# Performance work log

Measured on AMD Instinct MI355X. Metric: run time of the kernel, lower is better.

## Reference

```python
import jax, jax.numpy as jnp
import numpy as np

N_COMP = 8
N_BASIS = 16
N_FEATURES = 64
N_CAT = 8
N_CONT = 56
N_UNIQUE = 100
BATCH = 32768
T0, T1 = 0.0, 10.0
SEP = 1e-3  # constants.MIN_TRANSITION_POINT_SEP
SIGNS = np.array([1.0, -1.0, 1.0, -1.0, 1.0, -1.0, 1.0, -1.0], dtype=np.float32)
CONT_IDX = np.arange(N_CONT)
CAT_IDX = np.arange(N_CONT, N_FEATURES)


def _offset():
    # torch_inverse_softplus(avg_interval_per_feature)
    v = (T1 - T0) / N_COMP / (N_FEATURES + 1)
    return float(np.log(np.exp(v) - 1.0))


def setup_inputs():
    key = jax.random.key(0)
    ks = jax.random.split(key, 11)
    off = _offset()
    B = jax.random.normal(ks[0], (BATCH, N_CONT, N_BASIS), jnp.float32)
    codes = jax.random.randint(ks[1], (BATCH, N_CAT), 0, N_UNIQUE)
    B_cat = jax.nn.one_hot(codes, N_UNIQUE, dtype=jnp.float32).reshape(BATCH, N_CAT * N_UNIQUE)
    Wh = jax.random.normal(ks[2], (N_BASIS, N_CONT, N_COMP), jnp.float32) + off
    Wh_cat = jax.random.normal(ks[3], (N_CAT, N_UNIQUE, N_COMP), jnp.float32) + off
    bh = jax.random.normal(ks[4], (N_COMP,), jnp.float32) + off
    Wv = jax.random.normal(ks[5], (N_BASIS, N_CONT, N_COMP), jnp.float32)
    Wv_cat = jax.random.normal(ks[6], (N_CAT, N_UNIQUE, N_COMP), jnp.float32)
    bv = jax.random.normal(ks[7], (N_COMP,), jnp.float32)
    Wic = jax.random.normal(ks[8], (N_BASIS, N_CONT, 1), jnp.float32)
    Wic_cat = jax.random.normal(ks[9], (N_CAT, N_UNIQUE, 1), jnp.float32)
    bic = jax.random.normal(ks[10], (1,), jnp.float32)
    return {"B": B, "B_cat": B_cat, "Wh": Wh, "Wh_cat": Wh_cat, "bh": bh,
            "Wv": Wv, "Wv_cat": Wv_cat, "bv": bv,
            "Wic": Wic, "Wic_cat": Wic_cat, "bic": bic}


def _calculate_gams(B, B_cat, W, W_cat, bias, positive):
    # continuous: per-feature small matmul  (b,i,k) x (k,i,c) -> (b,c,i)
    cont = jnp.einsum('bik,kic->bci', B, W)
    # categorical: one-hot gather expressed as blockwise matmul  (b,f,n) x (f,n,c) -> (b,c,f)
    cat = jnp.einsum('bfn,fnc->bcf', B_cat.reshape(B.shape[0], N_CAT, N_UNIQUE), W_cat)
    c = W.shape[2]
    out = jnp.zeros((B.shape[0], c, N_FEATURES + 1), dtype=B.dtype)
    out = out.at[:, :, CONT_IDX].set(cont)
    out = out.at[:, :, CAT_IDX].set(cat)
    out = out.at[:, :, -1].set(bias[None, :])
    return jax.nn.softplus(out) if positive else out


def reference(B, B_cat, Wh, Wh_cat, bh, Wv, Wv_cat, bv, Wic, Wic_cat, bic):
    H = _calculate_gams(B, B_cat, Wh, Wh_cat, bh, True)      # (b, n_comp, n_feat+1)
    V = _calculate_gams(B, B_cat, Wv, Wv_cat, bv, True)      # (b, n_comp, n_feat+1)
    IC = _calculate_gams(B, B_cat, Wic, Wic_cat, bic, False)  # (b, 1, n_feat+1)
    b = B.shape[0]
    signs = jnp.asarray(SIGNS)
    h_sum = H.sum(-1)   # (b, n_comp) per-segment horizontal increments
    v_sum = V.sum(-1)
    sep = SEP * jnp.arange(1, N_COMP + 1, dtype=B.dtype)
    # sequential cumulative build == prefix sums over the composition axis
    t = jnp.concatenate([jnp.full((b, 1), T0, B.dtype),
                         T0 + jnp.cumsum(h_sum, axis=1) + sep], axis=1)  # (b, n_comp+1)
    x0 = IC.sum(-1)     # (b, 1)
    x = jnp.concatenate([x0, x0 + jnp.cumsum(signs * v_sum, axis=1)], axis=1)
    # bounded composition: clamp the last horizontal coordinate
    t = t.at[:, -1].set(jnp.maximum(t[:, -2] + SEP, T1))
    return jnp.stack([t, x], axis=-1)  # (b, n_comp+1, 2)
```

## Files before the change

kernel.cpp:

```cpp
#include <hip/hip_runtime.h>

#define NCOMP 8
#define NCONT 56
#define NCAT 8
#define NU 100
#define NROWS 32768
#define SEPC 1e-3f
#define T1F 10.0f

typedef __fp16 f16x2 __attribute__((ext_vector_type(2)));
typedef _Float16 h2arith __attribute__((ext_vector_type(2)));

#define FSTRIDE 35

union H8 { f16x2 h2[4]; float4 f4; };

__device__ __forceinline__ float sp(float x) {
    return 0.69314718f * __builtin_amdgcn_logf(1.0f + __builtin_amdgcn_exp2f(x * 1.44269504f));
}

__device__ __forceinline__ f16x2 pkrtz(float a, float b) {
    return __builtin_amdgcn_cvt_pkrtz(a, b);
}

__device__ __forceinline__ float fdot2(f16x2 a, f16x2 b, float c) {
    return __builtin_amdgcn_fdot2(a, b, c, false);
}

__device__ __forceinline__ h2arith h2shfl_xor(h2arith v, int off) {
    int i = __builtin_bit_cast(int, v);
    i = __shfl_xor(i, off, 64);
    return __builtin_bit_cast(h2arith, i);
}

__device__ __forceinline__ void acc_cont(const float4* __restrict__ pw,
                                         float4 a0, float4 a1, float4 a2, float4 a3,
                                         float* sh, float* sw, float& ic) {
    f16x2 ba[8];
    ba[0] = pkrtz(a0.x, a0.y); ba[1] = pkrtz(a0.z, a0.w);
    ba[2] = pkrtz(a1.x, a1.y); ba[3] = pkrtz(a1.z, a1.w);
    ba[4] = pkrtz(a2.x, a2.y); ba[5] = pkrtz(a2.z, a2.w);
    ba[6] = pkrtz(a3.x, a3.y); ba[7] = pkrtz(a3.z, a3.w);
#pragma unroll
    for (int c = 0; c < NCOMP; ++c) {
        H8 u0, u1, v0, v1;
        u0.f4 = pw[2 * c];      u1.f4 = pw[2 * c + 1];
        v0.f4 = pw[16 + 2 * c]; v1.f4 = pw[17 + 2 * c];
        float hA = 0.0f, vA = 0.0f;
#pragma unroll
        for (int p = 0; p < 4; ++p) {
            hA = fdot2(ba[p], u0.h2[p], hA);
            vA = fdot2(ba[p], v0.h2[p], vA);
        }
#pragma unroll
        for (int p = 0; p < 4; ++p) {
            hA = fdot2(ba[4 + p], u1.h2[p], hA);
            vA = fdot2(ba[4 + p], v1.h2[p], vA);
        }
        sh[c] += sp(hA);
        sw[c] += sp(vA);
    }
    H8 i0, i1;
    i0.f4 = pw[32]; i1.f4 = pw[33];
    float iA = 0.0f;
#pragma unroll
    for (int p = 0; p < 4; ++p) iA = fdot2(ba[p], i0.h2[p], iA);
#pragma unroll
    for (int p = 0; p < 4; ++p) iA = fdot2(ba[4 + p], i1.h2[p], iA);
    ic += iA;
}

__global__ __launch_bounds__(512, 4) void tpm_kernel(
    const float* __restrict__ B, const float* __restrict__ Bcat,
    const float* __restrict__ Wh, const float* __restrict__ Whc, const float* __restrict__ bh,
    const float* __restrict__ Wv, const float* __restrict__ Wvc, const float* __restrict__ bv,
    const float* __restrict__ Wic, const float* __restrict__ Wicc, const float* __restrict__ bic,
    float* __restrict__ out)
{
    __shared__ float4 sW[NCONT * FSTRIDE];
    __shared__ float2 sBias[NCOMP];
    __shared__ float  sBic;
    __shared__ int    sCode[8][4][NCAT];

    const int tid = threadIdx.x;

    for (int idx = tid; idx < 896; idx += 512) {
        int icp = idx % 448, t = idx / 448;
        int i = icp >> 3, c = icp & 7;
        const float* gh = Wh + (size_t)(8 * t) * 448 + icp;
        const float* gv = Wv + (size_t)(8 * t) * 448 + icp;
        H8 uh, uv;
#pragma unroll
        for (int p = 0; p < 4; ++p) {
            uh.h2[p] = pkrtz(gh[(2 * p) * 448], gh[(2 * p + 1) * 448]);
            uv.h2[p] = pkrtz(gv[(2 * p) * 448], gv[(2 * p + 1) * 448]);
        }
        sW[i * FSTRIDE + 2 * c + t] = uh.f4;
        sW[i * FSTRIDE + 16 + 2 * c + t] = uv.f4;
    }
    if (tid < 112) {
        int i = tid % 56, t = tid / 56;
        const float* gi = Wic + (size_t)(8 * t) * 56 + i;
        H8 u;
#pragma unroll
        for (int p = 0; p < 4; ++p)
            u.h2[p] = pkrtz(gi[(2 * p) * 56], gi[(2 * p + 1) * 56]);
        sW[i * FSTRIDE + 32 + t] = u.f4;
    }
    if (tid < NCOMP) sBias[tid] = make_float2(sp(bh[tid]), sp(bv[tid]));
    if (tid == NCOMP) sBic = bic[0];
    __syncthreads();

    const int lane = tid & 63;
    const int widx = tid >> 6;
    const int s = lane & 15;
    const int g = lane >> 4;
    const int R0 = (((blockIdx.x << 3) + widx) << 2);
    const int r = R0 + g;
    const float* browp = B + (size_t)r * 896;

    {
        const float4* pc = (const float4*)(Bcat + (size_t)R0 * 800);
#pragma unroll
        for (int it = 0; it < 13; ++it) {
            int idx = it * 64 + lane;
            if (it < 12 || idx < 800) {
                int row = idx / 200;
                int pos = idx - row * 200;
                float4 q = pc[idx];
                float n = (float)(4 * pos);
                float sc = q.x * (n + 1.0f) + q.y * (n + 2.0f) + q.z * (n + 3.0f) + q.w * (n + 4.0f);
                if (sc > 0.5f) {
                    int p = (int)sc - 1;
                    int f = p / NU;
                    sCode[widx][row][f] = p - f * NU;
                }
            }
        }
    }
    __threadfence_block();

    float4 p3a, p3b, p3c, p3d;
    float p3ic = 0.0f;
    if (s >= 8) {
        int fi = s - 8;
        int cc = sCode[widx][g][fi];
        int gA = fi * NU + cc;
        const float4* qh = (const float4*)(Whc + gA * 8);
        const float4* qv = (const float4*)(Wvc + gA * 8);
        p3a = qh[0]; p3b = qh[1]; p3c = qv[0]; p3d = qv[1];
        p3ic = Wicc[gA];
    }

    float sh[NCOMP], sw[NCOMP];
    float ic = 0.0f;
#pragma unroll
    for (int c = 0; c < NCOMP; ++c) { sh[c] = sw[c] = 0.0f; }

    float4 cb0, cb1, cb2, cb3;
    {
        const float4* p = (const float4*)(browp + s * 16);
        cb0 = p[0]; cb1 = p[1]; cb2 = p[2]; cb3 = p[3];
    }

#pragma unroll
    for (int j = 0; j < 3; ++j) {
        float4 nb0, nb1, nb2, nb3;
        if (j < 2) {
            const float4* p = (const float4*)(browp + (s + 16 * (j + 1)) * 16);
            nb0 = p[0]; nb1 = p[1]; nb2 = p[2]; nb3 = p[3];
        } else {
            int f3 = (s < 8) ? (s + 48) : 48;
            const float4* p = (const float4*)(browp + f3 * 16);
            nb0 = p[0]; nb1 = p[1]; nb2 = p[2]; nb3 = p[3];
        }
        acc_cont(sW + (s + 16 * j) * FSTRIDE, cb0, cb1, cb2, cb3, sh, sw, ic);
        cb0 = nb0; cb1 = nb1; cb2 = nb2; cb3 = nb3;
    }

    if (s < 8) {
        acc_cont(sW + (s + 48) * FSTRIDE, cb0, cb1, cb2, cb3, sh, sw, ic);
    } else {
        sh[0] += sp(p3a.x); sh[1] += sp(p3a.y); sh[2] += sp(p3a.z); sh[3] += sp(p3a.w);
        sh[4] += sp(p3b.x); sh[5] += sp(p3b.y); sh[6] += sp(p3b.z); sh[7] += sp(p3b.w);
        sw[0] += sp(p3c.x); sw[1] += sp(p3c.y); sw[2] += sp(p3c.z); sw[3] += sp(p3c.w);
        sw[4] += sp(p3d.x); sw[5] += sp(p3d.y); sw[6] += sp(p3d.z); sw[7] += sp(p3d.w);
        ic += p3ic;
    }

    h2arith hw[NCOMP];
#pragma unroll
    for (int c = 0; c < NCOMP; ++c)
        hw[c] = __builtin_bit_cast(h2arith, pkrtz(sh[c], sw[c]));
#pragma unroll
    for (int off = 8; off >= 1; off >>= 1) {
#pragma unroll
        for (int c = 0; c < NCOMP; ++c)
            hw[c] = hw[c] + h2shfl_xor(hw[c], off);
        ic += __shfl_xor(ic, off, 64);
    }

    if (s < 9) {
        int m = (s == 8) ? 7 : s;
        float tj = SEPC * (float)s;
        float xj = ic + sBic;
#pragma unroll
        for (int c = 0; c < NCOMP; ++c) {
            float2 bb2 = sBias[c];
            if (c < m) tj += (float)hw[c][0] + bb2.x;
            if (c < s) {
                float vv = (float)hw[c][1] + bb2.y;
                xj += (c & 1) ? -vv : vv;
            }
        }
        if (s == 8) tj = fmaxf(tj, T1F);
        float2 o; o.x = tj; o.y = xj;
        ((float2*)out)[(size_t)r * 9 + s] = o;
    }
}

extern "C" void kernel_launch(void* const* d_in, const int* in_sizes, int n_in,
                              void* d_out, int out_size, void* d_ws, size_t ws_size,
                              hipStream_t stream) {
    (void)in_sizes; (void)n_in; (void)out_size; (void)d_ws; (void)ws_size;
    const float* B    = (const float*)d_in[0];
    const float* Bcat = (const float*)d_in[1];
    const float* Wh   = (const float*)d_in[2];
    const float* Whc  = (const float*)d_in[3];
    const float* bh   = (const float*)d_in[4];
    const float* Wv   = (const float*)d_in[5];
    const float* Wvc  = (const float*)d_in[6];
    const float* bv   = (const float*)d_in[7];
    const float* Wic  = (const float*)d_in[8];
    const float* Wicc = (const float*)d_in[9];
    const float* bic  = (const float*)d_in[10];
    float* out = (float*)d_out;

    hipLaunchKernelGGL(tpm_kernel, dim3(1024), dim3(512), 0, stream,
                       B, Bcat, Wh, Whc, bh, Wv, Wvc, bv, Wic, Wicc, bic, out);
}
```

Measured before the change: 260.7 us.

## Precompute fp16 weight tiles in prep kernel and overlap Bcat scan with compute

Adds a small prep kernel that packs the continuous weights into fp16 float4 tiles and the softplus'd biases into the workspace once per call. Each block then just copies that packed layout into shared memory instead of gathering and converting strided weights itself. The one-hot Bcat loads and scan are issued early and interleaved with the continuous-feature accumulation, and the B row loads are software-pipelined. Inside acc_cont the weight reads from shared memory are double-buffered one component ahead. The cost is an extra kernel launch and higher register pressure from keeping many loads in flight.

```diff
diff --git a/kernel.cpp b/kernel.cpp
--- a/kernel.cpp
+++ b/kernel.cpp
@@ -4,14 +4,15 @@
 #define NCONT 56
 #define NCAT 8
 #define NU 100
-#define NROWS 32768
 #define SEPC 1e-3f
 #define T1F 10.0f
 
+#define FSTRIDE 35
+#define WS_NW4 2048
+#define WS_BIAS_OFF 32768
+
 typedef __fp16 f16x2 __attribute__((ext_vector_type(2)));
 typedef _Float16 h2arith __attribute__((ext_vector_type(2)));
-
-#define FSTRIDE 35
 
 union H8 { f16x2 h2[4]; float4 f4; };
 
@@ -41,11 +42,19 @@
     ba[2] = pkrtz(a1.x, a1.y); ba[3] = pkrtz(a1.z, a1.w);
     ba[4] = pkrtz(a2.x, a2.y); ba[5] = pkrtz(a2.z, a2.w);
     ba[6] = pkrtz(a3.x, a3.y); ba[7] = pkrtz(a3.z, a3.w);
+    H8 u0, u1, v0, v1;
+    u0.f4 = pw[0];  u1.f4 = pw[1];
+    v0.f4 = pw[16]; v1.f4 = pw[17];
 #pragma unroll
     for (int c = 0; c < NCOMP; ++c) {
-        H8 u0, u1, v0, v1;
-        u0.f4 = pw[2 * c];      u1.f4 = pw[2 * c + 1];
-        v0.f4 = pw[16 + 2 * c]; v1.f4 = pw[17 + 2 * c];
+        H8 nu0, nu1, nv0, nv1;
+        if (c < NCOMP - 1) {
+            nu0.f4 = pw[2 * c + 2];  nu1.f4 = pw[2 * c + 3];
+            nv0.f4 = pw[18 + 2 * c]; nv1.f4 = pw[19 + 2 * c];
+        } else {
+            nu0.f4 = pw[32]; nu1.f4 = pw[33];
+            nv0.f4 = u0.f4;  nv1.f4 = u1.f4;
+        }
         float hA = 0.0f, vA = 0.0f;
 #pragma unroll
         for (int p = 0; p < 4; ++p) {
@@ -59,58 +68,66 @@
         }
         sh[c] += sp(hA);
         sw[c] += sp(vA);
-    }
-    H8 i0, i1;
-    i0.f4 = pw[32]; i1.f4 = pw[33];
+        u0 = nu0; u1 = nu1; v0 = nv0; v1 = nv1;
+    }
     float iA = 0.0f;
 #pragma unroll
-    for (int p = 0; p < 4; ++p) iA = fdot2(ba[p], i0.h2[p], iA);
-#pragma unroll
-    for (int p = 0; p < 4; ++p) iA = fdot2(ba[4 + p], i1.h2[p], iA);
+    for (int p = 0; p < 4; ++p) iA = fdot2(ba[p], u0.h2[p], iA);
+#pragma unroll
+    for (int p = 0; p < 4; ++p) iA = fdot2(ba[4 + p], u1.h2[p], iA);
     ic += iA;
+}
+
+__global__ __launch_bounds__(512) void prep_kernel(
+    const float* __restrict__ Wh, const float* __restrict__ Wv,
+    const float* __restrict__ Wic, const float* __restrict__ bh,
+    const float* __restrict__ bv, const float* __restrict__ bic,
+    float4* __restrict__ ws)
+{
+    const int id = blockIdx.x * 512 + threadIdx.x;
+    const int i  = id / FSTRIDE;
+    const int rr = id - i * FSTRIDE;
+    H8 u;
+    u.f4 = make_float4(0.f, 0.f, 0.f, 0.f);
+    if (i < NCONT && rr < 34) {
+        if (rr < 32) {
+            const int c = (rr & 15) >> 1;
+            const int t = rr & 1;
+            const float* W  = (rr < 16) ? Wh : Wv;
+            const float* gp = W + (size_t)(8 * t) * 448 + i * 8 + c;
+#pragma unroll
+            for (int p = 0; p < 4; ++p)
+                u.h2[p] = pkrtz(gp[(2 * p) * 448], gp[(2 * p + 1) * 448]);
+        } else {
+            const int t = rr - 32;
+            const float* gp = Wic + (size_t)(8 * t) * 56 + i;
+#pragma unroll
+            for (int p = 0; p < 4; ++p)
+                u.h2[p] = pkrtz(gp[(2 * p) * 56], gp[(2 * p + 1) * 56]);
+        }
+    }
+    ws[id] = u.f4;
+    if (id < NCOMP) {
+        float2* b2 = (float2*)((char*)ws + WS_BIAS_OFF);
+        b2[id] = make_float2(sp(bh[id]), sp(bv[id]));
+    }
+    if (id == NCOMP) {
+        *((float*)((char*)ws + WS_BIAS_OFF + 64)) = bic[0];
+    }
 }
 
 __global__ __launch_bounds__(512, 4) void tpm_kernel(
     const float* __restrict__ B, const float* __restrict__ Bcat,
-    const float* __restrict__ Wh, const float* __restrict__ Whc, const float* __restrict__ bh,
-    const float* __restrict__ Wv, const float* __restrict__ Wvc, const float* __restrict__ bv,
-    const float* __restrict__ Wic, const float* __restrict__ Wicc, const float* __restrict__ bic,
+    const float* __restrict__ Whc, const float* __restrict__ Wvc,
+    const float* __restrict__ Wicc, const float4* __restrict__ ws,
     float* __restrict__ out)
 {
-    __shared__ float4 sW[NCONT * FSTRIDE];
+    __shared__ float4 sW[WS_NW4];
     __shared__ float2 sBias[NCOMP];
     __shared__ float  sBic;
     __shared__ int    sCode[8][4][NCAT];
 
-    const int tid = threadIdx.x;
-
-    for (int idx = tid; idx < 896; idx += 512) {
-        int icp = idx % 448, t = idx / 448;
-        int i = icp >> 3, c = icp & 7;
-        const float* gh = Wh + (size_t)(8 * t) * 448 + icp;
-        const float* gv = Wv + (size_t)(8 * t) * 448 + icp;
-        H8 uh, uv;
-#pragma unroll
-        for (int p = 0; p < 4; ++p) {
-            uh.h2[p] = pkrtz(gh[(2 * p) * 448], gh[(2 * p + 1) * 448]);
-            uv.h2[p] = pkrtz(gv[(2 * p) * 448], gv[(2 * p + 1) * 448]);
-        }
-        sW[i * FSTRIDE + 2 * c + t] = uh.f4;
-        sW[i * FSTRIDE + 16 + 2 * c + t] = uv.f4;
-    }
-    if (tid < 112) {
-        int i = tid % 56, t = tid / 56;
-        const float* gi = Wic + (size_t)(8 * t) * 56 + i;
-        H8 u;
-#pragma unroll
-        for (int p = 0; p < 4; ++p)
-            u.h2[p] = pkrtz(gi[(2 * p) * 56], gi[(2 * p + 1) * 56]);
-        sW[i * FSTRIDE + 32 + t] = u.f4;
-    }
-    if (tid < NCOMP) sBias[tid] = make_float2(sp(bh[tid]), sp(bv[tid]));
-    if (tid == NCOMP) sBic = bic[0];
-    __syncthreads();
-
+    const int tid  = threadIdx.x;
     const int lane = tid & 63;
     const int widx = tid >> 6;
     const int s = lane & 15;
@@ -118,26 +135,73 @@
     const int R0 = (((blockIdx.x << 3) + widx) << 2);
     const int r = R0 + g;
     const float* browp = B + (size_t)r * 896;
-
+    const float4* pcat = (const float4*)(Bcat + (size_t)R0 * 800);
+
+    float4 qa0 = pcat[lane];
+    float4 qa1 = pcat[64 + lane];
+    float4 qa2 = pcat[128 + lane];
+    float4 qa3 = pcat[192 + lane];
+    float4 cb0, cb1, cb2, cb3;
     {
-        const float4* pc = (const float4*)(Bcat + (size_t)R0 * 800);
-#pragma unroll
-        for (int it = 0; it < 13; ++it) {
-            int idx = it * 64 + lane;
-            if (it < 12 || idx < 800) {
-                int row = idx / 200;
-                int pos = idx - row * 200;
-                float4 q = pc[idx];
-                float n = (float)(4 * pos);
-                float sc = q.x * (n + 1.0f) + q.y * (n + 2.0f) + q.z * (n + 3.0f) + q.w * (n + 4.0f);
-                if (sc > 0.5f) {
-                    int p = (int)sc - 1;
-                    int f = p / NU;
-                    sCode[widx][row][f] = p - f * NU;
-                }
+        const float4* p = (const float4*)(browp + s * 16);
+        cb0 = p[0]; cb1 = p[1]; cb2 = p[2]; cb3 = p[3];
+    }
+
+#pragma unroll
+    for (int k = 0; k < 4; ++k) sW[tid + k * 512] = ws[tid + k * 512];
+    if (tid < NCOMP) sBias[tid] = ((const float2*)((const char*)ws + WS_BIAS_OFF))[tid];
+    if (tid == NCOMP) sBic = *((const float*)((const char*)ws + WS_BIAS_OFF + 64));
+    __syncthreads();
+
+    auto do_scan = [&](float4 q, int it) {
+        int idx = it * 64 + lane;
+        if (it < 12 || idx < 800) {
+            int row = idx / 200;
+            int pos = idx - row * 200;
+            float n = (float)(4 * pos);
+            float sc = q.x * (n + 1.0f) + q.y * (n + 2.0f) + q.z * (n + 3.0f) + q.w * (n + 4.0f);
+            if (sc > 0.5f) {
+                int p = (int)sc - 1;
+                int f = p / NU;
+                sCode[widx][row][f] = p - f * NU;
             }
         }
-    }
+    };
+
+    float sh[NCOMP], sw[NCOMP];
+    float ic = 0.0f;
+#pragma unroll
+    for (int c = 0; c < NCOMP; ++c) { sh[c] = sw[c] = 0.0f; }
+
+    float4 qb0 = pcat[256 + lane];
+    float4 qb1 = pcat[320 + lane];
+    float4 qb2 = pcat[384 + lane];
+    float4 qb3 = pcat[448 + lane];
+    float4 qb4 = pcat[512 + lane];
+    float4 nb0, nb1, nb2, nb3;
+    {
+        const float4* p = (const float4*)(browp + (s + 16) * 16);
+        nb0 = p[0]; nb1 = p[1]; nb2 = p[2]; nb3 = p[3];
+    }
+
+    do_scan(qa0, 0); do_scan(qa1, 1); do_scan(qa2, 2); do_scan(qa3, 3);
+    acc_cont(sW + s * FSTRIDE, cb0, cb1, cb2, cb3, sh, sw, ic);
+
+    float4 qc0 = pcat[576 + lane];
+    float4 qc1 = pcat[640 + lane];
+    float4 qc2 = pcat[704 + lane];
+    float4 qc3 = make_float4(0.f, 0.f, 0.f, 0.f);
+    if (lane < 32) qc3 = pcat[768 + lane];
+    float4 mb0, mb1, mb2, mb3;
+    {
+        const float4* p = (const float4*)(browp + (s + 32) * 16);
+        mb0 = p[0]; mb1 = p[1]; mb2 = p[2]; mb3 = p[3];
+    }
+
+    do_scan(qb0, 4); do_scan(qb1, 5); do_scan(qb2, 6); do_scan(qb3, 7); do_scan(qb4, 8);
+    acc_cont(sW + (s + 16) * FSTRIDE, nb0, nb1, nb2, nb3, sh, sw, ic);
+
+    do_scan(qc0, 9); do_scan(qc1, 10); do_scan(qc2, 11); do_scan(qc3, 12);
     __threadfence_block();
 
     float4 p3a, p3b, p3c, p3d;
@@ -151,35 +215,16 @@
         p3a = qh[0]; p3b = qh[1]; p3c = qv[0]; p3d = qv[1];
         p3ic = Wicc[gA];
     }
-
-    float sh[NCOMP], sw[NCOMP];
-    float ic = 0.0f;
-#pragma unroll
-    for (int c = 0; c < NCOMP; ++c) { sh[c] = sw[c] = 0.0f; }
-
-    float4 cb0, cb1, cb2, cb3;
-    {
-        const float4* p = (const float4*)(browp + s * 16);
-        cb0 = p[0]; cb1 = p[1]; cb2 = p[2]; cb3 = p[3];
-    }
-
-#pragma unroll
-    for (int j = 0; j < 3; ++j) {
-        float4 nb0, nb1, nb2, nb3;
-        if (j < 2) {
-            const float4* p = (const float4*)(browp + (s + 16 * (j + 1)) * 16);
-            nb0 = p[0]; nb1 = p[1]; nb2 = p[2]; nb3 = p[3];
-        } else {
-            int f3 = (s < 8) ? (s + 48) : 48;
-            const float4* p = (const float4*)(browp + f3 * 16);
-            nb0 = p[0]; nb1 = p[1]; nb2 = p[2]; nb3 = p[3];
-        }
-        acc_cont(sW + (s + 16 * j) * FSTRIDE, cb0, cb1, cb2, cb3, sh, sw, ic);
-        cb0 = nb0; cb1 = nb1; cb2 = nb2; cb3 = nb3;
-    }
-
+    float4 db0, db1, db2, db3;
     if (s < 8) {
-        acc_cont(sW + (s + 48) * FSTRIDE, cb0, cb1, cb2, cb3, sh, sw, ic);
+        const float4* p = (const float4*)(browp + (s + 48) * 16);
+        db0 = p[0]; db1 = p[1]; db2 = p[2]; db3 = p[3];
+    }
+
+    acc_cont(sW + (s + 32) * FSTRIDE, mb0, mb1, mb2, mb3, sh, sw, ic);
+
+    if (s < 8) {
+        acc_cont(sW + (s + 48) * FSTRIDE, db0, db1, db2, db3, sh, sw, ic);
     } else {
         sh[0] += sp(p3a.x); sh[1] += sp(p3a.y); sh[2] += sp(p3a.z); sh[3] += sp(p3a.w);
         sh[4] += sp(p3b.x); sh[5] += sp(p3b.y); sh[6] += sp(p3b.z); sh[7] += sp(p3b.w);
@@ -222,7 +267,7 @@
 extern "C" void kernel_launch(void* const* d_in, const int* in_sizes, int n_in,
                               void* d_out, int out_size, void* d_ws, size_t ws_size,
                               hipStream_t stream) {
-    (void)in_sizes; (void)n_in; (void)out_size; (void)d_ws; (void)ws_size;
+    (void)in_sizes; (void)n_in; (void)out_size; (void)ws_size;
     const float* B    = (const float*)d_in[0];
     const float* Bcat = (const float*)d_in[1];
     const float* Wh   = (const float*)d_in[2];
@@ -235,7 +280,10 @@
     const float* Wicc = (const float*)d_in[9];
     const float* bic  = (const float*)d_in[10];
     float* out = (float*)d_out;
-
+    float4* ws = (float4*)d_ws;
+
+    hipLaunchKernelGGL(prep_kernel, dim3(4), dim3(512), 0, stream,
+                       Wh, Wv, Wic, bh, bv, bic, ws);
     hipLaunchKernelGGL(tpm_kernel, dim3(1024), dim3(512), 0, stream,
-                       B, Bcat, Wh, Whc, bh, Wv, Wvc, bv, Wic, Wicc, bic, out);
-}
+                       B, Bcat, Whc, Wvc, Wicc, ws, out);
+}
```

New measurement: 469.8 us. 1.8x slower.
